# Kernel optimization log

Measured on AMD Instinct MI355X. Metric: run time of the kernel, lower is better.

## Reference

```python
import jax, jax.numpy as jnp
import numpy as np

N = 262144
FC = 256
XYZ_FREQ, DIR_FREQ = 10, 4
IN_XYZ = 3 + 3 * 2 * XYZ_FREQ  # 63
IN_DIR = 3 + 3 * 2 * DIR_FREQ  # 27
SKIP = 4


def posenc(p, n_freqs):
    bands = 2.0 ** jnp.arange(n_freqs, dtype=p.dtype)          # [F]
    xb = p[..., None, :] * bands[:, None]                       # [N, F, 3]
    sc = jnp.stack([jnp.sin(xb), jnp.cos(xb)], axis=-2)         # [N, F, 2, 3]
    return jnp.concatenate([p, sc.reshape(p.shape[0], n_freqs * 6)], axis=-1)


def setup_inputs() -> dict:
    key = jax.random.key(0)
    ks = jax.random.split(key, 32)
    s = 0.05
    inp = {"x": jax.random.normal(ks[0], (N, 6), jnp.float32)}
    dims_in = [IN_XYZ] + [FC + IN_XYZ if i == SKIP else FC for i in range(1, 8)]
    for i in range(8):
        inp[f"w{i}"] = jax.random.normal(ks[1 + i], (dims_in[i], FC), jnp.float32) * s
        inp[f"b{i}"] = jnp.zeros((FC,), jnp.float32)
    inp["w_final"] = jax.random.normal(ks[10], (FC, FC), jnp.float32) * s
    inp["b_final"] = jnp.zeros((FC,), jnp.float32)
    inp["w_sigma"] = jax.random.normal(ks[11], (FC, 1), jnp.float32) * s
    inp["b_sigma"] = jnp.zeros((1,), jnp.float32)
    inp["w_rgb1"] = jax.random.normal(ks[12], (FC + IN_DIR, FC // 2), jnp.float32) * s
    inp["b_rgb1"] = jnp.zeros((FC // 2,), jnp.float32)
    inp["w_rgb2"] = jax.random.normal(ks[13], (FC // 2, 3), jnp.float32) * s
    inp["b_rgb2"] = jnp.zeros((3,), jnp.float32)
    return inp


def reference(x, w0, b0, w1, b1, w2, b2, w3, b3, w4, b4, w5, b5, w6, b6, w7, b7,
              w_final, b_final, w_sigma, b_sigma, w_rgb1, b_rgb1, w_rgb2, b_rgb2):
    input_xyz = posenc(x[:, :3], XYZ_FREQ)   # [N, 63]
    input_dir = posenc(x[:, 3:], DIR_FREQ)   # [N, 27]
    ws = [w0, w1, w2, w3, w4, w5, w6, w7]
    bs = [b0, b1, b2, b3, b4, b5, b6, b7]
    h = input_xyz
    for i in range(8):
        if i == SKIP:
            h = jnp.concatenate([input_xyz, h], axis=-1)
        h = jax.nn.relu(h @ ws[i] + bs[i])
    sigma = h @ w_sigma + b_sigma                               # [N, 1]
    final = h @ w_final + b_final                               # [N, 256]
    dir_enc = jnp.concatenate([final, input_dir], axis=-1)      # [N, 283]
    hidden = jax.nn.relu(dir_enc @ w_rgb1 + b_rgb1)
    rgb = jax.nn.sigmoid(hidden @ w_rgb2 + b_rgb2)              # [N, 3]
    return jnp.concatenate([rgb, sigma], axis=-1)               # [N, 4]
```

## Files before the change

### kernel.cpp

```cpp
#include <hip/hip_runtime.h>
#include <hip/hip_fp16.h>
#include <stdint.h>

typedef unsigned int   uint32;
typedef unsigned short ushort_t;
typedef _Float16 half8   __attribute__((ext_vector_type(8)));
typedef float    floatx4 __attribute__((ext_vector_type(4)));

#define DEVINL __device__ __forceinline__

#define HSTR 264
#define XSTR 72
#define DSTR 40
#define N_FRAGS 1172

__device__ __align__(16) ushort_t g_ws[(size_t)N_FRAGS * 512];

DEVINL ushort_t f2h_u(float v) { return __half_as_ushort(__float2half(v)); }

DEVINL uint4 make_frag_qword(const float* __restrict__ W, int Kr, int Nr,
                             int skip63, int kt, int nt, int q, int cc)
{
    const int n = nt*16 + cc;
    uint32 pk[4];
    #pragma unroll
    for (int jj = 0; jj < 4; ++jj) {
        ushort_t h2[2];
        #pragma unroll
        for (int e = 0; e < 2; ++e) {
            const int k = kt*32 + q*8 + jj*2 + e;
            float v = 0.f;
            if (n < Nr) {
                if (skip63) {
                    if (k != 63) { const int rr = (k < 63) ? k : (k - 1); v = W[(size_t)rr*Nr + n]; }
                } else if (k < Kr) {
                    v = W[(size_t)k*Nr + n];
                }
            }
            h2[e] = f2h_u(v);
        }
        pk[jj] = (uint32)h2[0] | ((uint32)h2[1] << 16);
    }
    return make_uint4(pk[0], pk[1], pk[2], pk[3]);
}

__global__ __launch_bounds__(256) void prep_weights(
    const float* __restrict__ w0, const float* __restrict__ w1,
    const float* __restrict__ w2, const float* __restrict__ w3,
    const float* __restrict__ w4, const float* __restrict__ w5,
    const float* __restrict__ w6, const float* __restrict__ w7,
    const float* __restrict__ wf, const float* __restrict__ wsig,
    const float* __restrict__ wr1, const float* __restrict__ wr2)
{
    int gid  = blockIdx.x * 256 + threadIdx.x;
    int frag = gid >> 6;
    if (frag >= N_FRAGS) return;
    int lane = gid & 63;
    const int foff[13] = {0,32,160,288,416,576,704,832,960,1088,1096,1168,1172};
    const int NT[12]   = {16,16,16,16,16,16,16,16,16,1,8,1};
    const int KR[12]   = {63,256,256,256,319,256,256,256,256,256,283,128};
    const int NR[12]   = {256,256,256,256,256,256,256,256,256,1,128,3};
    const float* WP[12] = {w0,w1,w2,w3,w4,w5,w6,w7,wf,wsig,wr1,wr2};
    int t = 0;
    while (frag >= foff[t+1]) ++t;
    int fl = frag - foff[t];
    int nt = fl % NT[t];
    int kt = fl / NT[t];
    uint4 pk = make_frag_qword(WP[t], KR[t], NR[t], (t == 4) ? 1 : 0, kt, nt,
                               lane >> 4, lane & 15);
    *(uint4*)(g_ws + (size_t)frag*512 + lane*8) = pk;
}

template <int NT_W, int KT, int KT_SPLIT, int NTT, int S0, int S1>
DEVINL void run_layer(const ushort_t* __restrict__ wsrc,
                      const ushort_t* __restrict__ in0,
                      const ushort_t* __restrict__ in1,
                      int lane, int q, int cc, int nt_lo,
                      const floatx4 (&binit)[NT_W], floatx4 (&acc)[4][NT_W])
{
    half8 bfr[2][4];
    half8 afr[2][NT_W];

    auto loadk = [&](int kt, int buf) {
        #pragma unroll
        for (int rt = 0; rt < 4; ++rt) {
            const ushort_t* p = (kt < KT_SPLIT)
                ? in0 + (rt*16 + cc)*S0 + kt*32 + q*8
                : in1 + (rt*16 + cc)*S1 + (kt - KT_SPLIT)*32 + q*8;
            bfr[buf][rt] = *(const half8*)p;
        }
        const ushort_t* wb = wsrc + (size_t)(kt*NTT + nt_lo)*512 + lane*8;
        #pragma unroll
        for (int nt = 0; nt < NT_W; ++nt)
            afr[buf][nt] = *(const half8*)(wb + nt*512);
    };

    loadk(0, 0);
    #pragma unroll
    for (int kt = 0; kt < KT; ++kt) {
        const int cur = kt & 1;
        if (kt + 1 < KT) loadk(kt + 1, cur ^ 1);
        #pragma unroll
        for (int nt = 0; nt < NT_W; ++nt)
            #pragma unroll
            for (int rt = 0; rt < 4; ++rt)
                acc[rt][nt] = __builtin_amdgcn_mfma_f32_16x16x32_f16(
                    afr[cur][nt], bfr[cur][rt],
                    (kt == 0) ? binit[nt] : acc[rt][nt], 0, 0, 0);
    }
}

template <int NT_W, bool RELU>
DEVINL void epilogue_h(floatx4 (&acc)[4][NT_W], int nt_lo,
                       ushort_t* __restrict__ shh, int q, int cc)
{
    #pragma unroll
    for (int rt = 0; rt < 4; ++rt) {
        const int m = rt*16 + cc;
        #pragma unroll
        for (int nt = 0; nt < NT_W; ++nt) {
            const int n = (nt_lo + nt)*16 + q*4;
            floatx4 v = acc[rt][nt];
            if (RELU) {
                v.x = fmaxf(v.x, 0.f); v.y = fmaxf(v.y, 0.f);
                v.z = fmaxf(v.z, 0.f); v.w = fmaxf(v.w, 0.f);
            }
            uint2 u;
            u.x = __builtin_bit_cast(uint32, __builtin_amdgcn_cvt_pkrtz(v.x, v.y));
            u.y = __builtin_bit_cast(uint32, __builtin_amdgcn_cvt_pkrtz(v.z, v.w));
            *(uint2*)(shh + (size_t)m*HSTR + n) = u;
        }
    }
}

__global__ __launch_bounds__(256, 3) void nerf_fused(
    const float* __restrict__ x,
    const float* __restrict__ b0, const float* __restrict__ b1,
    const float* __restrict__ b2, const float* __restrict__ b3,
    const float* __restrict__ b4, const float* __restrict__ b5,
    const float* __restrict__ b6, const float* __restrict__ b7,
    const float* __restrict__ bf, const float* __restrict__ bsig,
    const float* __restrict__ br1, const float* __restrict__ br2,
    float* __restrict__ out)
{
    __shared__ __align__(16) ushort_t shh[64*HSTR];
    __shared__ __align__(16) ushort_t shx[64*XSTR];
    __shared__ __align__(16) ushort_t shd[64*DSTR];

    const int tid  = threadIdx.x;
    const int wave = tid >> 6, lane = tid & 63;
    const int q = lane >> 4, cc = lane & 15;
    const int r0 = blockIdx.x * 64;
    const ushort_t* ws = g_ws;

    {
        const int r = lane;
        const float* xr = x + (size_t)(r0 + r)*6;
        for (int j = wave; j < 42; j += 4) {
            if (j < 30) {
                int f = j/3, a = j%3;
                float v = xr[a] * (float)(1 << f);
                shx[r*XSTR + 3 + f*6 + a]     = f2h_u(sinf(v));
                shx[r*XSTR + 3 + f*6 + 3 + a] = f2h_u(cosf(v));
            } else {
                int jj = j - 30, f = jj/3, a = jj%3;
                float v = xr[3+a] * (float)(1 << f);
                shd[r*DSTR + 3 + f*6 + a]     = f2h_u(sinf(v));
                shd[r*DSTR + 3 + f*6 + 3 + a] = f2h_u(cosf(v));
            }
        }
        if (wave == 0) {
            #pragma unroll
            for (int a = 0; a < 3; ++a) {
                shx[r*XSTR + a] = f2h_u(xr[a]);
                shd[r*DSTR + a] = f2h_u(xr[3+a]);
            }
            shx[r*XSTR + 63] = 0;
            #pragma unroll
            for (int kq = 27; kq < 32; ++kq) shd[r*DSTR + kq] = 0;
        }
    }
    __syncthreads();

    const float* BS[8] = {b0,b1,b2,b3,b4,b5,b6,b7};
    const int WO[8] = {0,16384,81920,147456,212992,294912,360448,425984};
    const int nt_lo4 = wave * 4;
    const floatx4 vz = {0.f, 0.f, 0.f, 0.f};

    floatx4 acc[4][4];
    floatx4 bl[4];

    #pragma unroll
    for (int nt = 0; nt < 4; ++nt)
        bl[nt] = *(const floatx4*)(b0 + (nt_lo4 + nt)*16 + q*4);
    run_layer<4,2,2,16,XSTR,XSTR>(ws + WO[0], shx, shx, lane, q, cc, nt_lo4, bl, acc);
    epilogue_h<4,true>(acc, nt_lo4, shh, q, cc);
    __syncthreads();

    #pragma unroll
    for (int l = 1; l < 8; ++l) {
        #pragma unroll
        for (int nt = 0; nt < 4; ++nt)
            bl[nt] = *(const floatx4*)(BS[l] + (nt_lo4 + nt)*16 + q*4);
        if (l == 4)
            run_layer<4,10,2,16,XSTR,HSTR>(ws + WO[4], shx, shh, lane, q, cc, nt_lo4, bl, acc);
        else
            run_layer<4,8,8,16,HSTR,HSTR>(ws + WO[l], shh, shh, lane, q, cc, nt_lo4, bl, acc);
        __syncthreads();
        epilogue_h<4,true>(acc, nt_lo4, shh, q, cc);
        __syncthreads();
    }

    if (wave == 0) {
        floatx4 sacc[4][1];
        const floatx4 bz[1] = {vz};
        run_layer<1,8,8,1,HSTR,HSTR>(ws + 557056, shh, shh, lane, q, cc, 0, bz, sacc);
        if (q == 0) {
            const float bs_ = bsig[0];
            #pragma unroll
            for (int rt = 0; rt < 4; ++rt)
                out[(size_t)(r0 + rt*16 + cc)*4 + 3] = sacc[rt][0].x + bs_;
        }
    }

    #pragma unroll
    for (int nt = 0; nt < 4; ++nt)
        bl[nt] = *(const floatx4*)(bf + (nt_lo4 + nt)*16 + q*4);
    run_layer<4,8,8,16,HSTR,HSTR>(ws + 491520, shh, shh, lane, q, cc, nt_lo4, bl, acc);
    __syncthreads();
    epilogue_h<4,false>(acc, nt_lo4, shh, q, cc);
    __syncthreads();

    {
        floatx4 racc[4][2];
        floatx4 bl2[2];
        #pragma unroll
        for (int nt = 0; nt < 2; ++nt)
            bl2[nt] = *(const floatx4*)(br1 + (wave*2 + nt)*16 + q*4);
        run_layer<2,9,8,8,HSTR,DSTR>(ws + 561152, shh, shd, lane, q, cc, wave*2, bl2, racc);
        __syncthreads();
        epilogue_h<2,true>(racc, wave*2, shh, q, cc);
        __syncthreads();
    }

    if (wave == 0) {
        floatx4 cacc[4][1];
        const floatx4 bz[1] = {vz};
        run_layer<1,4,4,1,HSTR,HSTR>(ws + 598016, shh, shh, lane, q, cc, 0, bz, cacc);
        if (q == 0) {
            const float c0 = br2[0], c1 = br2[1], c2 = br2[2];
            #pragma unroll
            for (int rt = 0; rt < 4; ++rt) {
                const size_t o = (size_t)(r0 + rt*16 + cc)*4;
                out[o+0] = 1.f/(1.f + expf(-(cacc[rt][0].x + c0)));
                out[o+1] = 1.f/(1.f + expf(-(cacc[rt][0].y + c1)));
                out[o+2] = 1.f/(1.f + expf(-(cacc[rt][0].z + c2)));
            }
        }
    }
}

extern "C" void kernel_launch(void* const* d_in, const int* in_sizes, int n_in,
                              void* d_out, int out_size, void* d_ws, size_t ws_size,
                              hipStream_t stream)
{
    const float* x  = (const float*)d_in[0];
    const float* w0 = (const float*)d_in[1];  const float* b0 = (const float*)d_in[2];
    const float* w1 = (const float*)d_in[3];  const float* b1 = (const float*)d_in[4];
    const float* w2 = (const float*)d_in[5];  const float* b2 = (const float*)d_in[6];
    const float* w3 = (const float*)d_in[7];  const float* b3 = (const float*)d_in[8];
    const float* w4 = (const float*)d_in[9];  const float* b4 = (const float*)d_in[10];
    const float* w5 = (const float*)d_in[11]; const float* b5 = (const float*)d_in[12];
    const float* w6 = (const float*)d_in[13]; const float* b6 = (const float*)d_in[14];
    const float* w7 = (const float*)d_in[15]; const float* b7 = (const float*)d_in[16];
    const float* wf = (const float*)d_in[17]; const float* bf = (const float*)d_in[18];
    const float* wsg= (const float*)d_in[19]; const float* bsg= (const float*)d_in[20];
    const float* wr1= (const float*)d_in[21]; const float* br1= (const float*)d_in[22];
    const float* wr2= (const float*)d_in[23]; const float* br2= (const float*)d_in[24];
    float* out = (float*)d_out;
    const int N = in_sizes[0] / 6;

    prep_weights<<<(N_FRAGS*64 + 255)/256, 256, 0, stream>>>(
        w0,w1,w2,w3,w4,w5,w6,w7,wf,wsg,wr1,wr2);
    nerf_fused<<<N/64, 256, 0, stream>>>(
        x, b0,b1,b2,b3,b4,b5,b6,b7, bf,bsg, br1,br2, out);
}
```

Before: 383.2 us.

## Prefetch next layer's weight fragments across barriers with triple-buffered A loads

Weight fragments now sit in a three-deep register ring, loaded two k-steps ahead. The first two fragments and the biases of the next layer are issued before the barrier and epilogue of the current layer, so global-load latency overlaps the synchronisation. __syncthreads is replaced by an LDS-only waitcnt plus s_barrier, so outstanding global loads stay in flight across barriers. The weight-prep kernel also swaps its per-thread table arrays for a switch. The extra buffers raise VGPR pressure, which may cut occupancy.

```diff
diff --git a/kernel.cpp b/kernel.cpp
--- a/kernel.cpp
+++ b/kernel.cpp
@@ -17,6 +17,11 @@
 __device__ __align__(16) ushort_t g_ws[(size_t)N_FRAGS * 512];
 
 DEVINL ushort_t f2h_u(float v) { return __half_as_ushort(__float2half(v)); }
+
+DEVINL void bar_lgkm() {
+    asm volatile("s_waitcnt lgkmcnt(0)" ::: "memory");
+    __builtin_amdgcn_s_barrier();
+}
 
 DEVINL uint4 make_frag_qword(const float* __restrict__ W, int Kr, int Nr,
                              int skip63, int kt, int nt, int q, int cc)
@@ -56,32 +61,56 @@
     int frag = gid >> 6;
     if (frag >= N_FRAGS) return;
     int lane = gid & 63;
-    const int foff[13] = {0,32,160,288,416,576,704,832,960,1088,1096,1168,1172};
-    const int NT[12]   = {16,16,16,16,16,16,16,16,16,1,8,1};
-    const int KR[12]   = {63,256,256,256,319,256,256,256,256,256,283,128};
-    const int NR[12]   = {256,256,256,256,256,256,256,256,256,1,128,3};
-    const float* WP[12] = {w0,w1,w2,w3,w4,w5,w6,w7,wf,wsig,wr1,wr2};
+
+    constexpr int foff[13] = {0,32,160,288,416,576,704,832,960,1088,1096,1168,1172};
     int t = 0;
-    while (frag >= foff[t+1]) ++t;
-    int fl = frag - foff[t];
-    int nt = fl % NT[t];
-    int kt = fl / NT[t];
-    uint4 pk = make_frag_qword(WP[t], KR[t], NR[t], (t == 4) ? 1 : 0, kt, nt,
+    #pragma unroll
+    for (int i = 1; i <= 11; ++i) if (frag >= foff[i]) t = i;
+
+    const float* W; int fo, ntc, Kr, Nr;
+    switch (t) {
+        case 0:  W = w0;   fo = 0;    ntc = 16; Kr = 63;  Nr = 256; break;
+        case 1:  W = w1;   fo = 32;   ntc = 16; Kr = 256; Nr = 256; break;
+        case 2:  W = w2;   fo = 160;  ntc = 16; Kr = 256; Nr = 256; break;
+        case 3:  W = w3;   fo = 288;  ntc = 16; Kr = 256; Nr = 256; break;
+        case 4:  W = w4;   fo = 416;  ntc = 16; Kr = 319; Nr = 256; break;
+        case 5:  W = w5;   fo = 576;  ntc = 16; Kr = 256; Nr = 256; break;
+        case 6:  W = w6;   fo = 704;  ntc = 16; Kr = 256; Nr = 256; break;
+        case 7:  W = w7;   fo = 832;  ntc = 16; Kr = 256; Nr = 256; break;
+        case 8:  W = wf;   fo = 960;  ntc = 16; Kr = 256; Nr = 256; break;
+        case 9:  W = wsig; fo = 1088; ntc = 1;  Kr = 256; Nr = 1;   break;
+        case 10: W = wr1;  fo = 1096; ntc = 8;  Kr = 283; Nr = 128; break;
+        default: W = wr2;  fo = 1168; ntc = 1;  Kr = 128; Nr = 3;   break;
+    }
+    int fl = frag - fo;
+    int nt = fl % ntc;
+    int kt = fl / ntc;
+    uint4 pk = make_frag_qword(W, Kr, Nr, (t == 4) ? 1 : 0, kt, nt,
                                lane >> 4, lane & 15);
     *(uint4*)(g_ws + (size_t)frag*512 + lane*8) = pk;
 }
 
-template <int NT_W, int KT, int KT_SPLIT, int NTT, int S0, int S1>
+template <int NT_W, int NTT>
+DEVINL void loadA(const ushort_t* __restrict__ wsrc, int kt, int nt_lo, int lane,
+                  half8 (&dst)[4])
+{
+    const ushort_t* wb = wsrc + (size_t)(kt*NTT + nt_lo)*512 + (size_t)lane*8;
+    #pragma unroll
+    for (int nt = 0; nt < NT_W; ++nt)
+        dst[nt] = *(const half8*)(wb + nt*512);
+}
+
+template <int NT_W, int KT, int KT_SPLIT, int NTT, int S0, int S1, int NPRE>
 DEVINL void run_layer(const ushort_t* __restrict__ wsrc,
                       const ushort_t* __restrict__ in0,
                       const ushort_t* __restrict__ in1,
                       int lane, int q, int cc, int nt_lo,
-                      const floatx4 (&binit)[NT_W], floatx4 (&acc)[4][NT_W])
+                      const floatx4 (&binit)[NT_W], floatx4 (&acc)[4][NT_W],
+                      half8 (&afr)[3][4])
 {
     half8 bfr[2][4];
-    half8 afr[2][NT_W];
-
-    auto loadk = [&](int kt, int buf) {
+
+    auto loadB = [&](int kt, int buf) {
         #pragma unroll
         for (int rt = 0; rt < 4; ++rt) {
             const ushort_t* p = (kt < KT_SPLIT)
@@ -89,23 +118,21 @@
                 : in1 + (rt*16 + cc)*S1 + (kt - KT_SPLIT)*32 + q*8;
             bfr[buf][rt] = *(const half8*)p;
         }
-        const ushort_t* wb = wsrc + (size_t)(kt*NTT + nt_lo)*512 + lane*8;
-        #pragma unroll
-        for (int nt = 0; nt < NT_W; ++nt)
-            afr[buf][nt] = *(const half8*)(wb + nt*512);
     };
 
-    loadk(0, 0);
+    if (NPRE < 1) loadA<NT_W,NTT>(wsrc, 0, nt_lo, lane, afr[0]);
+    if (KT > 1 && NPRE < 2) loadA<NT_W,NTT>(wsrc, 1, nt_lo, lane, afr[1]);
+    loadB(0, 0);
     #pragma unroll
     for (int kt = 0; kt < KT; ++kt) {
-        const int cur = kt & 1;
-        if (kt + 1 < KT) loadk(kt + 1, cur ^ 1);
+        if (kt + 1 < KT) loadB(kt + 1, (kt + 1) & 1);
+        if (kt + 2 < KT) loadA<NT_W,NTT>(wsrc, kt + 2, nt_lo, lane, afr[(kt + 2) % 3]);
         #pragma unroll
         for (int nt = 0; nt < NT_W; ++nt)
             #pragma unroll
             for (int rt = 0; rt < 4; ++rt)
                 acc[rt][nt] = __builtin_amdgcn_mfma_f32_16x16x32_f16(
-                    afr[cur][nt], bfr[cur][rt],
+                    afr[kt % 3][nt], bfr[kt & 1][rt],
                     (kt == 0) ? binit[nt] : acc[rt][nt], 0, 0, 0);
     }
 }
@@ -152,6 +179,15 @@
     const int q = lane >> 4, cc = lane & 15;
     const int r0 = blockIdx.x * 64;
     const ushort_t* ws = g_ws;
+    const int nt_lo4 = wave * 4;
+
+    half8 afr[3][4];
+    loadA<4,16>(ws, 0, nt_lo4, lane, afr[0]);
+    loadA<4,16>(ws, 1, nt_lo4, lane, afr[1]);
+    floatx4 bl[4];
+    #pragma unroll
+    for (int nt = 0; nt < 4; ++nt)
+        bl[nt] = *(const floatx4*)(b0 + (nt_lo4 + nt)*16 + q*4);
 
     {
         const int r = lane;
@@ -180,41 +216,47 @@
             for (int kq = 27; kq < 32; ++kq) shd[r*DSTR + kq] = 0;
         }
     }
-    __syncthreads();
+    bar_lgkm();
 
     const float* BS[8] = {b0,b1,b2,b3,b4,b5,b6,b7};
     const int WO[8] = {0,16384,81920,147456,212992,294912,360448,425984};
-    const int nt_lo4 = wave * 4;
     const floatx4 vz = {0.f, 0.f, 0.f, 0.f};
 
     floatx4 acc[4][4];
-    floatx4 bl[4];
-
+
+    run_layer<4,2,2,16,XSTR,XSTR,2>(ws + WO[0], shx, shx, lane, q, cc, nt_lo4, bl, acc, afr);
+    loadA<4,16>(ws + WO[1], 0, nt_lo4, lane, afr[0]);
+    loadA<4,16>(ws + WO[1], 1, nt_lo4, lane, afr[1]);
     #pragma unroll
     for (int nt = 0; nt < 4; ++nt)
-        bl[nt] = *(const floatx4*)(b0 + (nt_lo4 + nt)*16 + q*4);
-    run_layer<4,2,2,16,XSTR,XSTR>(ws + WO[0], shx, shx, lane, q, cc, nt_lo4, bl, acc);
+        bl[nt] = *(const floatx4*)(b1 + (nt_lo4 + nt)*16 + q*4);
+    bar_lgkm();
     epilogue_h<4,true>(acc, nt_lo4, shh, q, cc);
-    __syncthreads();
+    bar_lgkm();
 
     #pragma unroll
     for (int l = 1; l < 8; ++l) {
+        if (l == 4)
+            run_layer<4,10,2,16,XSTR,HSTR,2>(ws + WO[4], shx, shh, lane, q, cc, nt_lo4, bl, acc, afr);
+        else
+            run_layer<4,8,8,16,HSTR,HSTR,2>(ws + WO[l], shh, shh, lane, q, cc, nt_lo4, bl, acc, afr);
+        const ushort_t* nw = (l < 7) ? ws + WO[l+1] : ws + 491520;
+        const float*    nb = (l < 7) ? BS[l+1] : bf;
+        loadA<4,16>(nw, 0, nt_lo4, lane, afr[0]);
+        loadA<4,16>(nw, 1, nt_lo4, lane, afr[1]);
         #pragma unroll
         for (int nt = 0; nt < 4; ++nt)
-            bl[nt] = *(const floatx4*)(BS[l] + (nt_lo4 + nt)*16 + q*4);
-        if (l == 4)
-            run_layer<4,10,2,16,XSTR,HSTR>(ws + WO[4], shx, shh, lane, q, cc, nt_lo4, bl, acc);
-        else
-            run_layer<4,8,8,16,HSTR,HSTR>(ws + WO[l], shh, shh, lane, q, cc, nt_lo4, bl, acc);
-        __syncthreads();
+            bl[nt] = *(const floatx4*)(nb + (nt_lo4 + nt)*16 + q*4);
+        bar_lgkm();
         epilogue_h<4,true>(acc, nt_lo4, shh, q, cc);
-        __syncthreads();
+        bar_lgkm();
     }
 
     if (wave == 0) {
+        half8 hfr[3][4];
         floatx4 sacc[4][1];
         const floatx4 bz[1] = {vz};
-        run_layer<1,8,8,1,HSTR,HSTR>(ws + 557056, shh, shh, lane, q, cc, 0, bz, sacc);
+        run_layer<1,8,8,1,HSTR,HSTR,0>(ws + 557056, shh, shh, lane, q, cc, 0, bz, sacc, hfr);
         if (q == 0) {
             const float bs_ = bsig[0];
             #pragma unroll
@@ -223,30 +265,30 @@
         }
     }
 
-    #pragma unroll
-    for (int nt = 0; nt < 4; ++nt)
-        bl[nt] = *(const floatx4*)(bf + (nt_lo4 + nt)*16 + q*4);
-    run_layer<4,8,8,16,HSTR,HSTR>(ws + 491520, shh, shh, lane, q, cc, nt_lo4, bl, acc);
-    __syncthreads();
+    run_layer<4,8,8,16,HSTR,HSTR,2>(ws + 491520, shh, shh, lane, q, cc, nt_lo4, bl, acc, afr);
+    loadA<2,8>(ws + 561152, 0, wave*2, lane, afr[0]);
+    loadA<2,8>(ws + 561152, 1, wave*2, lane, afr[1]);
+    floatx4 bl2[2];
+    #pragma unroll
+    for (int nt = 0; nt < 2; ++nt)
+        bl2[nt] = *(const floatx4*)(br1 + (wave*2 + nt)*16 + q*4);
+    bar_lgkm();
     epilogue_h<4,false>(acc, nt_lo4, shh, q, cc);
-    __syncthreads();
+    bar_lgkm();
 
     {
         floatx4 racc[4][2];
-        floatx4 bl2[2];
-        #pragma unroll
-        for (int nt = 0; nt < 2; ++nt)
-            bl2[nt] = *(const floatx4*)(br1 + (wave*2 + nt)*16 + q*4);
-        run_layer<2,9,8,8,HSTR,DSTR>(ws + 561152, shh, shd, lane, q, cc, wave*2, bl2, racc);
-        __syncthreads();
+        run_layer<2,9,8,8,HSTR,DSTR,2>(ws + 561152, shh, shd, lane, q, cc, wave*2, bl2, racc, afr);
+        bar_lgkm();
         epilogue_h<2,true>(racc, wave*2, shh, q, cc);
-        __syncthreads();
+        bar_lgkm();
     }
 
     if (wave == 0) {
+        half8 hfr[3][4];
         floatx4 cacc[4][1];
         const floatx4 bz[1] = {vz};
-        run_layer<1,4,4,1,HSTR,HSTR>(ws + 598016, shh, shh, lane, q, cc, 0, bz, cacc);
+        run_layer<1,4,4,1,HSTR,HSTR,0>(ws + 598016, shh, shh, lane, q, cc, 0, bz, cacc, hfr);
         if (q == 0) {
             const float c0 = br2[0], c1 = br2[1], c2 = br2[2];
             #pragma unroll
```

After: 434.3 us. 13.3% more time.

## Store activations in MFMA fragment-native LDS layout for contiguous per-lane loads

Applied to the files above, without the earlier changes.

Replaces the row-major padded LDS activation buffers with a fragment-tiled layout, so each lane reads its B operand as one contiguous 16-byte chunk at lane*8 with simple offsets. The epilogue and the positional-encoding writers scatter into the same tiled layout. The goals are fewer address computations and conflict-free LDS reads. The prep kernel also replaces its runtime table lookups with a switch. The risk is bank conflicts on the scattered uint2 epilogue stores.

```diff
diff --git a/kernel.cpp b/kernel.cpp
--- a/kernel.cpp
+++ b/kernel.cpp
@@ -9,10 +9,11 @@
 
 #define DEVINL __device__ __forceinline__
 
-#define HSTR 264
-#define XSTR 72
-#define DSTR 40
 #define N_FRAGS 1172
+
+DEVINL int fragoff(int row, int f) {
+    return (f >> 5)*2048 + (row >> 4)*512 + ((f >> 3) & 3)*128 + (row & 15)*8 + (f & 7);
+}
 
 __device__ __align__(16) ushort_t g_ws[(size_t)N_FRAGS * 512];
 
@@ -56,39 +57,51 @@
     int frag = gid >> 6;
     if (frag >= N_FRAGS) return;
     int lane = gid & 63;
-    const int foff[13] = {0,32,160,288,416,576,704,832,960,1088,1096,1168,1172};
-    const int NT[12]   = {16,16,16,16,16,16,16,16,16,1,8,1};
-    const int KR[12]   = {63,256,256,256,319,256,256,256,256,256,283,128};
-    const int NR[12]   = {256,256,256,256,256,256,256,256,256,1,128,3};
-    const float* WP[12] = {w0,w1,w2,w3,w4,w5,w6,w7,wf,wsig,wr1,wr2};
+
+    constexpr int foff[13] = {0,32,160,288,416,576,704,832,960,1088,1096,1168,1172};
     int t = 0;
-    while (frag >= foff[t+1]) ++t;
-    int fl = frag - foff[t];
-    int nt = fl % NT[t];
-    int kt = fl / NT[t];
-    uint4 pk = make_frag_qword(WP[t], KR[t], NR[t], (t == 4) ? 1 : 0, kt, nt,
+    #pragma unroll
+    for (int i = 1; i <= 11; ++i) if (frag >= foff[i]) t = i;
+
+    const float* W; int fo, ntc, Kr, Nr;
+    switch (t) {
+        case 0:  W = w0;   fo = 0;    ntc = 16; Kr = 63;  Nr = 256; break;
+        case 1:  W = w1;   fo = 32;   ntc = 16; Kr = 256; Nr = 256; break;
+        case 2:  W = w2;   fo = 160;  ntc = 16; Kr = 256; Nr = 256; break;
+        case 3:  W = w3;   fo = 288;  ntc = 16; Kr = 256; Nr = 256; break;
+        case 4:  W = w4;   fo = 416;  ntc = 16; Kr = 319; Nr = 256; break;
+        case 5:  W = w5;   fo = 576;  ntc = 16; Kr = 256; Nr = 256; break;
+        case 6:  W = w6;   fo = 704;  ntc = 16; Kr = 256; Nr = 256; break;
+        case 7:  W = w7;   fo = 832;  ntc = 16; Kr = 256; Nr = 256; break;
+        case 8:  W = wf;   fo = 960;  ntc = 16; Kr = 256; Nr = 256; break;
+        case 9:  W = wsig; fo = 1088; ntc = 1;  Kr = 256; Nr = 1;   break;
+        case 10: W = wr1;  fo = 1096; ntc = 8;  Kr = 283; Nr = 128; break;
+        default: W = wr2;  fo = 1168; ntc = 1;  Kr = 128; Nr = 3;   break;
+    }
+    int fl = frag - fo;
+    int nt = fl % ntc;
+    int kt = fl / ntc;
+    uint4 pk = make_frag_qword(W, Kr, Nr, (t == 4) ? 1 : 0, kt, nt,
                                lane >> 4, lane & 15);
     *(uint4*)(g_ws + (size_t)frag*512 + lane*8) = pk;
 }
 
-template <int NT_W, int KT, int KT_SPLIT, int NTT, int S0, int S1>
+template <int NT_W, int KT, int KT_SPLIT, int NTT>
 DEVINL void run_layer(const ushort_t* __restrict__ wsrc,
                       const ushort_t* __restrict__ in0,
                       const ushort_t* __restrict__ in1,
-                      int lane, int q, int cc, int nt_lo,
+                      int lane, int nt_lo,
                       const floatx4 (&binit)[NT_W], floatx4 (&acc)[4][NT_W])
 {
     half8 bfr[2][4];
     half8 afr[2][NT_W];
 
     auto loadk = [&](int kt, int buf) {
-        #pragma unroll
-        for (int rt = 0; rt < 4; ++rt) {
-            const ushort_t* p = (kt < KT_SPLIT)
-                ? in0 + (rt*16 + cc)*S0 + kt*32 + q*8
-                : in1 + (rt*16 + cc)*S1 + (kt - KT_SPLIT)*32 + q*8;
-            bfr[buf][rt] = *(const half8*)p;
-        }
+        const ushort_t* bb = ((kt < KT_SPLIT) ? in0 + kt*2048
+                                              : in1 + (kt - KT_SPLIT)*2048) + lane*8;
+        #pragma unroll
+        for (int rt = 0; rt < 4; ++rt)
+            bfr[buf][rt] = *(const half8*)(bb + rt*512);
         const ushort_t* wb = wsrc + (size_t)(kt*NTT + nt_lo)*512 + lane*8;
         #pragma unroll
         for (int nt = 0; nt < NT_W; ++nt)
@@ -112,14 +125,13 @@
 
 template <int NT_W, bool RELU>
 DEVINL void epilogue_h(floatx4 (&acc)[4][NT_W], int nt_lo,
-                       ushort_t* __restrict__ shh, int q, int cc)
+                       ushort_t* __restrict__ dsth, int q, int cc)
 {
     #pragma unroll
     for (int rt = 0; rt < 4; ++rt) {
-        const int m = rt*16 + cc;
         #pragma unroll
         for (int nt = 0; nt < NT_W; ++nt) {
-            const int n = (nt_lo + nt)*16 + q*4;
+            const int ng = nt_lo + nt;
             floatx4 v = acc[rt][nt];
             if (RELU) {
                 v.x = fmaxf(v.x, 0.f); v.y = fmaxf(v.y, 0.f);
@@ -128,7 +140,9 @@
             uint2 u;
             u.x = __builtin_bit_cast(uint32, __builtin_amdgcn_cvt_pkrtz(v.x, v.y));
             u.y = __builtin_bit_cast(uint32, __builtin_amdgcn_cvt_pkrtz(v.z, v.w));
-            *(uint2*)(shh + (size_t)m*HSTR + n) = u;
+            const int dst = (ng >> 1)*2048 + rt*512
+                          + (((2*ng + (q >> 1)) & 3)*16 + cc)*8 + (q & 1)*4;
+            *(uint2*)(dsth + dst) = u;
         }
     }
 }
@@ -143,9 +157,9 @@
     const float* __restrict__ br1, const float* __restrict__ br2,
     float* __restrict__ out)
 {
-    __shared__ __align__(16) ushort_t shh[64*HSTR];
-    __shared__ __align__(16) ushort_t shx[64*XSTR];
-    __shared__ __align__(16) ushort_t shd[64*DSTR];
+    __shared__ __align__(16) ushort_t shh[8*2048];
+    __shared__ __align__(16) ushort_t shx[2*2048];
+    __shared__ __align__(16) ushort_t shd[2048];
 
     const int tid  = threadIdx.x;
     const int wave = tid >> 6, lane = tid & 63;
@@ -160,24 +174,24 @@
             if (j < 30) {
                 int f = j/3, a = j%3;
                 float v = xr[a] * (float)(1 << f);
-                shx[r*XSTR + 3 + f*6 + a]     = f2h_u(sinf(v));
-                shx[r*XSTR + 3 + f*6 + 3 + a] = f2h_u(cosf(v));
+                shx[fragoff(r, 3 + f*6 + a)]     = f2h_u(sinf(v));
+                shx[fragoff(r, 3 + f*6 + 3 + a)] = f2h_u(cosf(v));
             } else {
                 int jj = j - 30, f = jj/3, a = jj%3;
                 float v = xr[3+a] * (float)(1 << f);
-                shd[r*DSTR + 3 + f*6 + a]     = f2h_u(sinf(v));
-                shd[r*DSTR + 3 + f*6 + 3 + a] = f2h_u(cosf(v));
+                shd[fragoff(r, 3 + f*6 + a)]     = f2h_u(sinf(v));
+                shd[fragoff(r, 3 + f*6 + 3 + a)] = f2h_u(cosf(v));
             }
         }
         if (wave == 0) {
             #pragma unroll
             for (int a = 0; a < 3; ++a) {
-                shx[r*XSTR + a] = f2h_u(xr[a]);
-                shd[r*DSTR + a] = f2h_u(xr[3+a]);
-            }
-            shx[r*XSTR + 63] = 0;
-            #pragma unroll
-            for (int kq = 27; kq < 32; ++kq) shd[r*DSTR + kq] = 0;
+                shx[fragoff(r, a)] = f2h_u(xr[a]);
+                shd[fragoff(r, a)] = f2h_u(xr[3+a]);
+            }
+            shx[fragoff(r, 63)] = 0;
+            #pragma unroll
+            for (int kq = 27; kq < 32; ++kq) shd[fragoff(r, kq)] = 0;
         }
     }
     __syncthreads();
@@ -193,7 +207,7 @@
     #pragma unroll
     for (int nt = 0; nt < 4; ++nt)
         bl[nt] = *(const floatx4*)(b0 + (nt_lo4 + nt)*16 + q*4);
-    run_layer<4,2,2,16,XSTR,XSTR>(ws + WO[0], shx, shx, lane, q, cc, nt_lo4, bl, acc);
+    run_layer<4,2,2,16>(ws + WO[0], shx, shx, lane, nt_lo4, bl, acc);
     epilogue_h<4,true>(acc, nt_lo4, shh, q, cc);
     __syncthreads();
 
@@ -203,9 +217,9 @@
         for (int nt = 0; nt < 4; ++nt)
             bl[nt] = *(const floatx4*)(BS[l] + (nt_lo4 + nt)*16 + q*4);
         if (l == 4)
-            run_layer<4,10,2,16,XSTR,HSTR>(ws + WO[4], shx, shh, lane, q, cc, nt_lo4, bl, acc);
+            run_layer<4,10,2,16>(ws + WO[4], shx, shh, lane, nt_lo4, bl, acc);
         else
-            run_layer<4,8,8,16,HSTR,HSTR>(ws + WO[l], shh, shh, lane, q, cc, nt_lo4, bl, acc);
+            run_layer<4,8,8,16>(ws + WO[l], shh, shh, lane, nt_lo4, bl, acc);
         __syncthreads();
         epilogue_h<4,true>(acc, nt_lo4, shh, q, cc);
         __syncthreads();
@@ -214,7 +228,7 @@
     if (wave == 0) {
         floatx4 sacc[4][1];
         const floatx4 bz[1] = {vz};
-        run_layer<1,8,8,1,HSTR,HSTR>(ws + 557056, shh, shh, lane, q, cc, 0, bz, sacc);
+        run_layer<1,8,8,1>(ws + 557056, shh, shh, lane, 0, bz, sacc);
         if (q == 0) {
             const float bs_ = bsig[0];
             #pragma unroll
@@ -226,7 +240,7 @@
     #pragma unroll
     for (int nt = 0; nt < 4; ++nt)
         bl[nt] = *(const floatx4*)(bf + (nt_lo4 + nt)*16 + q*4);
-    run_layer<4,8,8,16,HSTR,HSTR>(ws + 491520, shh, shh, lane, q, cc, nt_lo4, bl, acc);
+    run_layer<4,8,8,16>(ws + 491520, shh, shh, lane, nt_lo4, bl, acc);
     __syncthreads();
     epilogue_h<4,false>(acc, nt_lo4, shh, q, cc);
     __syncthreads();
@@ -237,7 +251,7 @@
         #pragma unroll
         for (int nt = 0; nt < 2; ++nt)
             bl2[nt] = *(const floatx4*)(br1 + (wave*2 + nt)*16 + q*4);
-        run_layer<2,9,8,8,HSTR,DSTR>(ws + 561152, shh, shd, lane, q, cc, wave*2, bl2, racc);
+        run_layer<2,9,8,8>(ws + 561152, shh, shd, lane, wave*2, bl2, racc);
         __syncthreads();
         epilogue_h<2,true>(racc, wave*2, shh, q, cc);
         __syncthreads();
@@ -246,7 +260,7 @@
     if (wave == 0) {
         floatx4 cacc[4][1];
         const floatx4 bz[1] = {vz};
-        run_layer<1,4,4,1,HSTR,HSTR>(ws + 598016, shh, shh, lane, q, cc, 0, bz, cacc);
+        run_layer<1,4,4,1>(ws + 598016, shh, shh, lane, 0, bz, cacc);
         if (q == 0) {
             const float c0 = br2[0], c1 = br2[1], c2 = br2[2];
             #pragma unroll
```

After: 384.0 us. About the same (+0.2%).
